# Optimization experiments

Hardware: AMD Instinct MI355X
Metric: run time of the kernel (lower is better)

The kernel has to match this reference:

```python
import jax, jax.numpy as jnp
import numpy as np

BATCH, NUM_FRAMES, FFT_SIZE = 256, 256, 512

def setup_inputs() -> dict:
    key = jax.random.key(0)
    k1, k2 = jax.random.split(key)
    inputs = jax.random.normal(k1, (BATCH, NUM_FRAMES, FFT_SIZE), dtype=jnp.float32)
    # Hann-like window (cfg.win_fn is a fixed per-bin window of length fft_size)
    window_fn = (0.5 - 0.5 * jnp.cos(2.0 * jnp.pi * jnp.arange(FFT_SIZE, dtype=jnp.float32) / FFT_SIZE))
    return {"inputs": inputs, "window_fn": window_fn}

def reference(inputs, window_fn):
    # window each frame, FFT along last axis (norm='backward' is jnp default), keep real part
    spec = jnp.fft.fft(inputs * window_fn, axis=-1).real.astype(jnp.float32)
    # output shape (batch, num_frames, fft_size, 1) as in the original reshape
    return spec[..., None]
```

## Files before the change

kernel.cpp:

```cpp
#include <hip/hip_runtime.h>
#include <math.h>

#define FFT_N 512
#define ROWS_PER_BLOCK 4
#define LDS_STRIDE 576

__device__ __forceinline__ void fft8(float* re, float* im) {
    const float C = 0.70710678118654752440f;
    float tr[8], ti[8];
    tr[0]=re[0]+re[4]; ti[0]=im[0]+im[4];
    tr[4]=re[0]-re[4]; ti[4]=im[0]-im[4];
    tr[1]=re[1]+re[5]; ti[1]=im[1]+im[5];
    tr[5]=re[1]-re[5]; ti[5]=im[1]-im[5];
    tr[2]=re[2]+re[6]; ti[2]=im[2]+im[6];
    tr[6]=re[2]-re[6]; ti[6]=im[2]-im[6];
    tr[3]=re[3]+re[7]; ti[3]=im[3]+im[7];
    tr[7]=re[3]-re[7]; ti[7]=im[3]-im[7];
    { float a=tr[5], b=ti[5]; tr[5]=C*(a+b); ti[5]=C*(b-a); }
    { float a=tr[6], b=ti[6]; tr[6]=b;       ti[6]=-a;      }
    { float a=tr[7], b=ti[7]; tr[7]=C*(b-a); ti[7]=-C*(a+b);}
    {
        float s0r=tr[0]+tr[2], s0i=ti[0]+ti[2];
        float s2r=tr[0]-tr[2], s2i=ti[0]-ti[2];
        float s1r=tr[1]+tr[3], s1i=ti[1]+ti[3];
        float dr =tr[1]-tr[3], di =ti[1]-ti[3];
        float s3r= di, s3i=-dr;
        re[0]=s0r+s1r; im[0]=s0i+s1i;
        re[2]=s2r+s3r; im[2]=s2i+s3i;
        re[4]=s0r-s1r; im[4]=s0i-s1i;
        re[6]=s2r-s3r; im[6]=s2i-s3i;
    }
    {
        float s0r=tr[4]+tr[6], s0i=ti[4]+ti[6];
        float s2r=tr[4]-tr[6], s2i=ti[4]-ti[6];
        float s1r=tr[5]+tr[7], s1i=ti[5]+ti[7];
        float dr =tr[5]-tr[7], di =ti[5]-ti[7];
        float s3r= di, s3i=-dr;
        re[1]=s0r+s1r; im[1]=s0i+s1i;
        re[3]=s2r+s3r; im[3]=s2i+s3i;
        re[5]=s0r-s1r; im[5]=s0i-s1i;
        re[7]=s2r-s3r; im[7]=s2i-s3i;
    }
}

__global__ __launch_bounds__(256) void fft512_r8_kernel(
        const float* __restrict__ x,
        const float* __restrict__ win,
        float* __restrict__ out) {
    __shared__ float lre[ROWS_PER_BLOCK * LDS_STRIDE];
    __shared__ float lim[ROWS_PER_BLOCK * LDS_STRIDE];

    const int wave = threadIdx.x >> 6;
    const int lane = threadIdx.x & 63;
    const int row  = blockIdx.x * ROWS_PER_BLOCK + wave;
    float* __restrict__ Lre = lre + wave * LDS_STRIDE;
    float* __restrict__ Lim = lim + wave * LDS_STRIDE;

    const float* __restrict__ xr = x + (size_t)row * FFT_N;
    float re[8], im[8];

#pragma unroll
    for (int n1 = 0; n1 < 8; ++n1) {
        re[n1] = xr[lane + 64 * n1] * win[lane + 64 * n1];
        im[n1] = 0.0f;
    }

    fft8(re, im);
#pragma unroll
    for (int k1 = 1; k1 < 8; ++k1) {
        float s, c;
        __sincosf(-6.283185307179586f * (float)(lane * k1) * (1.0f / 512.0f), &s, &c);
        float a = re[k1], b = im[k1];
        re[k1] = a * c - b * s;
        im[k1] = a * s + b * c;
    }

#pragma unroll
    for (int k1 = 0; k1 < 8; ++k1) {
        Lre[k1 * 72 + lane] = re[k1];
        Lim[k1 * 72 + lane] = im[k1];
    }
    __syncthreads();
    const int k1p = lane >> 3, n3p = lane & 7;
#pragma unroll
    for (int n2 = 0; n2 < 8; ++n2) {
        re[n2] = Lre[k1p * 72 + n2 * 8 + n3p];
        im[n2] = Lim[k1p * 72 + n2 * 8 + n3p];
    }

    fft8(re, im);
#pragma unroll
    for (int k2 = 1; k2 < 8; ++k2) {
        float s, c;
        __sincosf(-6.283185307179586f * (float)(n3p * k2) * (1.0f / 64.0f), &s, &c);
        float a = re[k2], b = im[k2];
        re[k2] = a * c - b * s;
        im[k2] = a * s + b * c;
    }
    __syncthreads();

#pragma unroll
    for (int k2 = 0; k2 < 8; ++k2) {
        int a = (k1p * 8 + k2) * 9 + n3p;
        Lre[a] = re[k2];
        Lim[a] = im[k2];
    }
    __syncthreads();
    const int k1pp = lane & 7, k2pp = lane >> 3;
#pragma unroll
    for (int n3 = 0; n3 < 8; ++n3) {
        int a = (k1pp * 8 + k2pp) * 9 + n3;
        re[n3] = Lre[a];
        im[n3] = Lim[a];
    }

    fft8(re, im);
    float* __restrict__ orow = out + (size_t)row * FFT_N;
#pragma unroll
    for (int k3 = 0; k3 < 8; ++k3) {
        orow[lane + 64 * k3] = re[k3];
    }
}

extern "C" void kernel_launch(void* const* d_in, const int* in_sizes, int n_in,
                              void* d_out, int out_size, void* d_ws, size_t ws_size,
                              hipStream_t stream) {
    const float* x   = (const float*)d_in[0];
    const float* win = (const float*)d_in[1];
    float* out       = (float*)d_out;

    const int rows   = in_sizes[0] / FFT_N;
    const int blocks = rows / ROWS_PER_BLOCK;
    hipLaunchKernelGGL(fft512_r8_kernel, dim3(blocks), dim3(256), 0, stream,
                       x, win, out);
}
```

Before: 228.3 us.

## Pack two real rows per complex FFT and use wave-local LDS sync

Each wavefront now handles two real rows packed as the real and imaginary parts of one complex FFT. The real part of each row's spectrum is recovered with a conjugate-symmetric gather through LDS. This halves the FFT work per row and halves the block count. Block-wide __syncthreads are replaced with wave-local barriers plus an LDS waitcnt, since each wave only touches its own LDS slice. Per-element sincos calls are replaced by a complex-multiply twiddle recurrence, and LDS uses interleaved float2, at the cost of an extra LDS round trip and slightly more rounding error.

```diff
diff --git a/kernel.cpp b/kernel.cpp
--- a/kernel.cpp
+++ b/kernel.cpp
@@ -2,8 +2,14 @@
 #include <math.h>
 
 #define FFT_N 512
-#define ROWS_PER_BLOCK 4
+#define WAVES_PER_BLOCK 4
 #define LDS_STRIDE 576
+
+#define WAVE_LDS_SYNC() do { \
+    __builtin_amdgcn_wave_barrier(); \
+    asm volatile("s_waitcnt lgkmcnt(0)" ::: "memory"); \
+    __builtin_amdgcn_wave_barrier(); \
+} while (0)
 
 __device__ __forceinline__ void fft8(float* re, float* im) {
     const float C = 0.70710678118654752440f;
@@ -43,82 +49,98 @@
     }
 }
 
-__global__ __launch_bounds__(256) void fft512_r8_kernel(
+__device__ __forceinline__ void twiddle_chain(float* re, float* im,
+                                              float c, float s) {
+    float cr = c, ci = s;
+#pragma unroll
+    for (int k = 1; k < 8; ++k) {
+        float a = re[k], b = im[k];
+        re[k] = a * cr - b * ci;
+        im[k] = a * ci + b * cr;
+        float ncr = cr * c - ci * s;
+        float nci = cr * s + ci * c;
+        cr = ncr; ci = nci;
+    }
+}
+
+__global__ __launch_bounds__(256) void fft512_pack2_kernel(
         const float* __restrict__ x,
         const float* __restrict__ win,
         float* __restrict__ out) {
-    __shared__ float lre[ROWS_PER_BLOCK * LDS_STRIDE];
-    __shared__ float lim[ROWS_PER_BLOCK * LDS_STRIDE];
+    __shared__ float2 lds[WAVES_PER_BLOCK * LDS_STRIDE];
 
     const int wave = threadIdx.x >> 6;
     const int lane = threadIdx.x & 63;
-    const int row  = blockIdx.x * ROWS_PER_BLOCK + wave;
-    float* __restrict__ Lre = lre + wave * LDS_STRIDE;
-    float* __restrict__ Lim = lim + wave * LDS_STRIDE;
+    const int pair = blockIdx.x * WAVES_PER_BLOCK + wave;
+    float2* __restrict__ L = lds + wave * LDS_STRIDE;
 
-    const float* __restrict__ xr = x + (size_t)row * FFT_N;
+    const float* __restrict__ x0 = x + (size_t)(2 * pair) * FFT_N;
+    const float* __restrict__ x1 = x0 + FFT_N;
+
     float re[8], im[8];
 
 #pragma unroll
     for (int n1 = 0; n1 < 8; ++n1) {
-        re[n1] = xr[lane + 64 * n1] * win[lane + 64 * n1];
-        im[n1] = 0.0f;
+        const int idx = lane + 64 * n1;
+        const float w = win[idx];
+        re[n1] = x0[idx] * w;
+        im[n1] = x1[idx] * w;
     }
 
     fft8(re, im);
-#pragma unroll
-    for (int k1 = 1; k1 < 8; ++k1) {
+    {
         float s, c;
-        __sincosf(-6.283185307179586f * (float)(lane * k1) * (1.0f / 512.0f), &s, &c);
-        float a = re[k1], b = im[k1];
-        re[k1] = a * c - b * s;
-        im[k1] = a * s + b * c;
+        __sincosf(-6.283185307179586f * (float)lane * (1.0f / 512.0f), &s, &c);
+        twiddle_chain(re, im, c, s);
     }
 
 #pragma unroll
-    for (int k1 = 0; k1 < 8; ++k1) {
-        Lre[k1 * 72 + lane] = re[k1];
-        Lim[k1 * 72 + lane] = im[k1];
-    }
-    __syncthreads();
+    for (int k1 = 0; k1 < 8; ++k1)
+        L[k1 * 72 + lane] = make_float2(re[k1], im[k1]);
+    WAVE_LDS_SYNC();
     const int k1p = lane >> 3, n3p = lane & 7;
 #pragma unroll
     for (int n2 = 0; n2 < 8; ++n2) {
-        re[n2] = Lre[k1p * 72 + n2 * 8 + n3p];
-        im[n2] = Lim[k1p * 72 + n2 * 8 + n3p];
+        float2 v = L[k1p * 72 + n2 * 8 + n3p];
+        re[n2] = v.x; im[n2] = v.y;
+    }
+    WAVE_LDS_SYNC();
+
+    fft8(re, im);
+    {
+        float s, c;
+        __sincosf(-6.283185307179586f * (float)n3p * (1.0f / 64.0f), &s, &c);
+        twiddle_chain(re, im, c, s);
     }
 
-    fft8(re, im);
 #pragma unroll
-    for (int k2 = 1; k2 < 8; ++k2) {
-        float s, c;
-        __sincosf(-6.283185307179586f * (float)(n3p * k2) * (1.0f / 64.0f), &s, &c);
-        float a = re[k2], b = im[k2];
-        re[k2] = a * c - b * s;
-        im[k2] = a * s + b * c;
-    }
-    __syncthreads();
-
-#pragma unroll
-    for (int k2 = 0; k2 < 8; ++k2) {
-        int a = (k1p * 8 + k2) * 9 + n3p;
-        Lre[a] = re[k2];
-        Lim[a] = im[k2];
-    }
-    __syncthreads();
+    for (int k2 = 0; k2 < 8; ++k2)
+        L[(k1p * 8 + k2) * 9 + n3p] = make_float2(re[k2], im[k2]);
+    WAVE_LDS_SYNC();
     const int k1pp = lane & 7, k2pp = lane >> 3;
 #pragma unroll
     for (int n3 = 0; n3 < 8; ++n3) {
-        int a = (k1pp * 8 + k2pp) * 9 + n3;
-        re[n3] = Lre[a];
-        im[n3] = Lim[a];
+        float2 v = L[(k1pp * 8 + k2pp) * 9 + n3];
+        re[n3] = v.x; im[n3] = v.y;
     }
+    WAVE_LDS_SYNC();
 
     fft8(re, im);
-    float* __restrict__ orow = out + (size_t)row * FFT_N;
+
+#pragma unroll
+    for (int k3 = 0; k3 < 8; ++k3)
+        L[k3 * 72 + lane] = make_float2(re[k3], im[k3]);
+    WAVE_LDS_SYNC();
+
+    float* __restrict__ o0 = out + (size_t)(2 * pair) * FFT_N;
+    float* __restrict__ o1 = o0 + FFT_N;
 #pragma unroll
     for (int k3 = 0; k3 < 8; ++k3) {
-        orow[lane + 64 * k3] = re[k3];
+        const int k  = lane + 64 * k3;
+        const int kk = (FFT_N - k) & (FFT_N - 1);
+        float2 p = L[(kk >> 6) * 72 + (kk & 63)];
+        o0[k] = 0.5f * (re[k3] + p.x);
+        o1[k] = 0.5f * (im[k3] + p.y);
     }
 }
 
@@ -130,7 +152,8 @@
     float* out       = (float*)d_out;
 
     const int rows   = in_sizes[0] / FFT_N;
-    const int blocks = rows / ROWS_PER_BLOCK;
-    hipLaunchKernelGGL(fft512_r8_kernel, dim3(blocks), dim3(256), 0, stream,
+    const int pairs  = rows / 2;
+    const int blocks = pairs / WAVES_PER_BLOCK;
+    hipLaunchKernelGGL(fft512_pack2_kernel, dim3(blocks), dim3(256), 0, stream,
                        x, win, out);
 }
```

Result: no change. 226.6 us (-0.7%).
